# Performance work log

Measured on AMD Instinct MI355X. Metric: run time of the kernel, lower is better.

## Reference

```python
import jax, jax.numpy as jnp
import numpy as np

B, C, H, W = 8, 256, 128, 128
CQK = C // 8  # query/key channels from 1x1 conv
NEG = -jnp.inf


def setup_inputs() -> dict:
    key = jax.random.key(0)
    ks = jax.random.split(key, 9)
    s = 0.05
    return {
        "x1": jax.random.normal(ks[0], (B, C, H, W), jnp.float32),
        "x2": jax.random.normal(ks[1], (B, C, H, W), jnp.float32),
        "Wq": jax.random.normal(ks[2], (CQK, C), jnp.float32) * s,
        "bq": jax.random.normal(ks[3], (CQK,), jnp.float32) * s,
        "Wk": jax.random.normal(ks[4], (CQK, C), jnp.float32) * s,
        "bk": jax.random.normal(ks[5], (CQK,), jnp.float32) * s,
        "Wv": jax.random.normal(ks[6], (C, C), jnp.float32) * s,
        "bv": jax.random.normal(ks[7], (C,), jnp.float32) * s,
        "gamma": jnp.ones((1,), jnp.float32),
    }


def _topk_mask(e, k):
    # keep top-k entries along last axis, set the rest to -inf
    vals = jax.lax.top_k(e, k)[0]
    thr = vals[..., -1:]
    return jnp.where(e >= thr, e, NEG)


def reference(x1, x2, Wq, bq, Wk, bk, Wv, bv, gamma):
    b, c, h, w = x1.shape
    # 1x1 convs == per-pixel linear maps over channels
    q = jnp.einsum('bchw,oc->bohw', x1, Wq) + bq[None, :, None, None]
    k = jnp.einsum('bchw,oc->bohw', x2, Wk) + bk[None, :, None, None]
    v = jnp.einsum('bchw,oc->bohw', x2, Wv) + bv[None, :, None, None]

    # column (H-axis) scores: for pixel (h,w), attend over all h' in same column w
    eH = jnp.einsum('bchw,bcgw->bhwg', q, k)                     # (B,H,W,H)
    eye = jnp.eye(h, dtype=bool)[None, :, None, :]               # mask self on H-axis
    eH = jnp.where(eye, NEG, eH)
    # row (W-axis) scores: attend over all w' in same row h
    eW = jnp.einsum('bchw,bchv->bhwv', q, k)                     # (B,H,W,W)

    # top-k sparsification along each axis (keep top half)
    eH = _topk_mask(eH, h // 2)
    eW = _topk_mask(eW, w // 2)

    att = jax.nn.softmax(jnp.concatenate([eH, eW], axis=-1), axis=-1)  # (B,H,W,H+W)
    attH, attW = att[..., :h], att[..., h:]

    outH = jnp.einsum('bcgw,bhwg->bchw', v, attH)
    outW = jnp.einsum('bchv,bhwv->bchw', v, attW)
    return gamma[0] * (outH + outW) + x1
```

## Files before the change

### kernel.cpp

```cpp
#include <hip/hip_runtime.h>
#include <cstdint>
#include <cstddef>

#define HW 16384
#define NEGF (-__builtin_inff())

typedef unsigned short u16;
typedef _Float16 f16;
typedef _Float16 f16x8 __attribute__((ext_vector_type(8)));
typedef float f32x4 __attribute__((ext_vector_type(4)));

__device__ __forceinline__ unsigned fkey(float f) {
  unsigned b = __float_as_uint(f);
  return (b & 0x80000000u) ? ~b : (b | 0x80000000u);
}
__device__ __forceinline__ float funkey(unsigned u) {
  unsigned b = (u & 0x80000000u) ? (u ^ 0x80000000u) : ~u;
  return __uint_as_float(b);
}

__device__ __forceinline__ float h2f(u16 u) { f16 h; *(u16*)&h = u; return (float)h; }
__device__ __forceinline__ u16 f2h(float f) { f16 h = (f16)f; return *(u16*)&h; }

union i4h8 { int4 i; f16x8 h; };

__global__ __launch_bounds__(256) void pack_kernel(
    const float* __restrict__ Wq, const float* __restrict__ bq,
    const float* __restrict__ Wk, const float* __restrict__ bk,
    const float* __restrict__ Wv, const float* __restrict__ bv,
    u16* __restrict__ Wp, float* __restrict__ ball)
{
  int i = blockIdx.x * 256 + threadIdx.x;
  {
    int chunk = i / 10240;
    int r = i - chunk * 10240;
    int frag = r >> 9;
    int lane = (r >> 3) & 63;
    int j = i & 7;
    int o = frag * 16 + (lane & 15);
    int kk = chunk * 32 + (lane >> 4) * 8 + j;
    float wv_ = (o < 32) ? Wq[o * 256 + kk]
              : (o < 64) ? Wk[(o - 32) * 256 + kk]
                         : Wv[(o - 64) * 256 + kk];
    Wp[i] = f2h(wv_);
  }
  if (i < 320) {
    ball[i] = (i < 32) ? bq[i] : (i < 64) ? bk[i - 32] : bv[i - 64];
  }
}

__global__ __launch_bounds__(256) void proj_kernel(
    const float* __restrict__ x1, const float* __restrict__ x2,
    const u16* __restrict__ Wp, const float* __restrict__ ball,
    u16* __restrict__ q16, u16* __restrict__ k16, u16* __restrict__ v)
{
  __shared__ __align__(16) char smem[42496];
  u16* wlds = (u16*)smem;
  u16* xlds0 = (u16*)(smem + 20480);
  u16* xlds1 = (u16*)(smem + 24576);

  const int t = threadIdx.x;
  const int w = t >> 6, l = t & 63;
  const int l15 = l & 15, l4 = l >> 4;
  const int blk = blockIdx.x;
  const int b = blk >> 8;
  const int p0 = (blk & 255) << 6;

  f32x4 acc[5][4];
#pragma unroll
  for (int f = 0; f < 5; ++f) {
    f32x4 binit;
#pragma unroll
    for (int r = 0; r < 4; ++r)
      binit[r] = ball[(w * 5 + f) * 16 + l4 * 4 + r];
#pragma unroll
    for (int pf = 0; pf < 4; ++pf) acc[f][pf] = binit;
  }

  const float* xp = (w & 1) ? x2 : x1;
  const int ks_l = (w >> 1) * 16 + (l >> 5) * 8;
  const int px_w = (l & 31) * 2;
  char* xdst = (char*)((w & 1) ? xlds1 : xlds0);
  const int kgw = ks_l >> 3;
  const int offA = px_w * 64 + ((kgw ^ (px_w & 3)) << 4);
  const int offB = (px_w + 1) * 64 + ((kgw ^ ((px_w + 1) & 3)) << 4);

  const int prow = l15, kg2 = l4;
  const char* xsrc1 = (const char*)xlds0;
  const char* xsrc2 = (const char*)xlds1;

  for (int ch = 0; ch < 8; ++ch) {
    int4 wreg[5];
#pragma unroll
    for (int r = 0; r < 5; ++r)
      wreg[r] = *(const int4*)((const char*)Wp + ch * 20480 + (r * 256 + t) * 16);
    float2 xv[8];
    {
      size_t gbase = ((size_t)(b * 256 + ch * 32 + ks_l)) * HW + p0 + px_w;
#pragma unroll
      for (int i = 0; i < 8; ++i) xv[i] = *(const float2*)&xp[gbase + (size_t)i * HW];
    }
    __syncthreads();
#pragma unroll
    for (int r = 0; r < 5; ++r)
      *(int4*)((char*)wlds + (r * 256 + t) * 16) = wreg[r];
    {
      union { u16 h[8]; int4 v4; } pk0, pk1;
#pragma unroll
      for (int i = 0; i < 8; ++i) {
        pk0.h[i] = f2h(xv[i].x); pk1.h[i] = f2h(xv[i].y);
      }
      *(int4*)(xdst + offA) = pk0.v4;
      *(int4*)(xdst + offB) = pk1.v4;
    }
    __syncthreads();

    f16x8 af[5];
#pragma unroll
    for (int f = 0; f < 5; ++f)
      af[f] = *(const f16x8*)((const char*)wlds + (((w * 5 + f) * 64 + l) << 4));
    f16x8 bf[4];
#pragma unroll
    for (int pf = 0; pf < 4; ++pf) {
      int row = pf * 16 + prow;
      bf[pf] = *(const f16x8*)(xsrc2 + row * 64 + ((kg2 ^ (row & 3)) << 4));
    }
    if (w == 0) {
#pragma unroll
      for (int f = 2; f < 5; ++f)
#pragma unroll
        for (int pf = 0; pf < 4; ++pf)
          acc[f][pf] = __builtin_amdgcn_mfma_f32_16x16x32_f16(af[f], bf[pf], acc[f][pf], 0, 0, 0);
#pragma unroll
      for (int pf = 0; pf < 4; ++pf) {
        int row = pf * 16 + prow;
        bf[pf] = *(const f16x8*)(xsrc1 + row * 64 + ((kg2 ^ (row & 3)) << 4));
      }
#pragma unroll
      for (int f = 0; f < 2; ++f)
#pragma unroll
        for (int pf = 0; pf < 4; ++pf)
          acc[f][pf] = __builtin_amdgcn_mfma_f32_16x16x32_f16(af[f], bf[pf], acc[f][pf], 0, 0, 0);
    } else {
#pragma unroll
      for (int f = 0; f < 5; ++f)
#pragma unroll
        for (int pf = 0; pf < 4; ++pf)
          acc[f][pf] = __builtin_amdgcn_mfma_f32_16x16x32_f16(af[f], bf[pf], acc[f][pf], 0, 0, 0);
    }
  }

  __syncthreads();
  u16* vs2 = (u16*)smem;
  u16* qks = (u16*)(smem + 33280);
#pragma unroll
  for (int f = 0; f < 5; ++f) {
    int of = w * 5 + f;
    if (of >= 4) {
      int cb = (of - 4) * 16 + l4 * 4;
#pragma unroll
      for (int pf = 0; pf < 4; ++pf) {
        ushort4 h4;
        h4.x = f2h(acc[f][pf][0]); h4.y = f2h(acc[f][pf][1]);
        h4.z = f2h(acc[f][pf][2]); h4.w = f2h(acc[f][pf][3]);
        *(ushort4*)&vs2[(pf * 16 + l15) * 260 + cb] = h4;
      }
    } else {
      int ob = (of & 1) * 16 + l4 * 4;
      int selo = (of >> 1) * 2304;
#pragma unroll
      for (int pf = 0; pf < 4; ++pf) {
        ushort4 h4;
        h4.x = f2h(acc[f][pf][0]); h4.y = f2h(acc[f][pf][1]);
        h4.z = f2h(acc[f][pf][2]); h4.w = f2h(acc[f][pf][3]);
        *(ushort4*)&qks[selo + (pf * 16 + l15) * 36 + ob] = h4;
      }
    }
  }
  __syncthreads();
  {
    const int c = t;
    u16* dst = v + ((size_t)b * 256 + c) * HW + p0;
#pragma unroll
    for (int g8 = 0; g8 < 8; ++g8) {
      union { u16 h[8]; int4 i; } u;
#pragma unroll
      for (int j = 0; j < 8; ++j) u.h[j] = vs2[(g8 * 8 + j) * 260 + c];
      *(int4*)&dst[g8 * 8] = u.i;
    }
  }
  if (t < 128) {
    const int sel = t >> 6, px = t & 63;
    const unsigned long long* sp =
        (const unsigned long long*)(qks + sel * 2304 + px * 36);
    u16* dst = (sel ? k16 : q16) + ((size_t)b * HW + p0 + px) * 32;
    union { unsigned long long u[8]; int4 i4[4]; } buf;
#pragma unroll
    for (int j = 0; j < 8; ++j) buf.u[j] = sp[j];
#pragma unroll
    for (int j = 0; j < 4; ++j) *(int4*)&dst[j * 8] = buf.i4[j];
  }
}

__global__ __launch_bounds__(256) void transpose_b16(
    const u16* __restrict__ in, u16* __restrict__ out)
{
  __shared__ u16 s[32][33];
  const int plane = blockIdx.y;
  const int tw = blockIdx.x & 3, th = blockIdx.x >> 2;
  const u16* ip = in + (size_t)plane * HW;
  u16* op = out + (size_t)plane * HW;
  const int lx = threadIdx.x & 31, ly = threadIdx.x >> 5;
  const int r0 = th << 5, c0 = tw << 5;
#pragma unroll
  for (int r = 0; r < 4; ++r) s[ly + 8 * r][lx] = ip[(r0 + ly + 8 * r) * 128 + c0 + lx];
  __syncthreads();
#pragma unroll
  for (int r = 0; r < 4; ++r) op[(c0 + ly + 8 * r) * 128 + r0 + lx] = s[lx][ly + 8 * r];
}

__global__ __launch_bounds__(256) void transpose_c32(
    const u16* __restrict__ in, u16* __restrict__ out)
{
  const int b = blockIdx.y;
  const int tw = blockIdx.x & 7, th = blockIdx.x >> 3;
  const int lw = threadIdx.x & 15, lh = threadIdx.x >> 4;
  const int h = th * 16 + lh, wc = tw * 16 + lw;
  const u16* src = in + ((size_t)b * HW + h * 128 + wc) * 32;
  u16* dst = out + ((size_t)b * HW + wc * 128 + h) * 32;
  int4 v0 = *(const int4*)&src[0];
  int4 v1 = *(const int4*)&src[8];
  int4 v2 = *(const int4*)&src[16];
  int4 v3 = *(const int4*)&src[24];
  *(int4*)&dst[0] = v0;  *(int4*)&dst[8] = v1;
  *(int4*)&dst[16] = v2; *(int4*)&dst[24] = v3;
}

__global__ __launch_bounds__(256) void stats_kernel(
    const u16* __restrict__ qp, const u16* __restrict__ kp,
    float* __restrict__ thr_out, float* __restrict__ m_out, float* __restrict__ l_out,
    int diag)
{
  __shared__ float q_s[32][132];
  __shared__ float k_s[32][132];
  __shared__ float e_s[32][132];
  const int t = threadIdx.x;
  const int po = blockIdx.x, b = blockIdx.y;

  const u16* qt = qp + (size_t)(b * 128 + po) * 128 * 32;
  const u16* kt = kp + (size_t)(b * 128 + po) * 128 * 32;
#pragma unroll
  for (int r = 0; r < 2; ++r) {
    int idx = t * 8 + r * 2048;
    int h = idx >> 5, c0 = idx & 31;
    i4h8 qv; qv.i = *(const int4*)&qt[idx];
    i4h8 kv; kv.i = *(const int4*)&kt[idx];
#pragma unroll
    for (int j = 0; j < 8; ++j) {
      q_s[c0 + j][h] = (float)qv.h[j];
      k_s[c0 + j][h] = (float)kv.h[j];
    }
  }
  __syncthreads();

  const int hh = t >> 3;
  const int gg0 = (t & 7) << 4;
  const int wv = t >> 6, ln = t & 63;

  for (int h0 = 0; h0 < 128; h0 += 32) {
    float acc[16];
#pragma unroll
    for (int j = 0; j < 16; ++j) acc[j] = 0.0f;
#pragma unroll
    for (int c = 0; c < 32; ++c) {
      float qv = q_s[c][h0 + hh];
      float4 kv[4];
      kv[0] = *(const float4*)&k_s[c][gg0];
      kv[1] = *(const float4*)&k_s[c][gg0 + 4];
      kv[2] = *(const float4*)&k_s[c][gg0 + 8];
      kv[3] = *(const float4*)&k_s[c][gg0 + 12];
#pragma unroll
      for (int j4 = 0; j4 < 4; ++j4) {
        acc[j4 * 4 + 0] = fmaf(qv, kv[j4].x, acc[j4 * 4 + 0]);
        acc[j4 * 4 + 1] = fmaf(qv, kv[j4].y, acc[j4 * 4 + 1]);
        acc[j4 * 4 + 2] = fmaf(qv, kv[j4].z, acc[j4 * 4 + 2]);
        acc[j4 * 4 + 3] = fmaf(qv, kv[j4].w, acc[j4 * 4 + 3]);
      }
    }
    if (diag) {
      int h = h0 + hh;
#pragma unroll
      for (int j = 0; j < 16; ++j)
        if (gg0 + j == h) acc[j] = NEGF;
    }
#pragma unroll
    for (int j4 = 0; j4 < 4; ++j4)
      *(float4*)&e_s[hh][gg0 + j4 * 4] =
          make_float4(acc[j4 * 4 + 0], acc[j4 * 4 + 1], acc[j4 * 4 + 2], acc[j4 * 4 + 3]);
    __syncthreads();

    for (int rr = 0; rr < 8; ++rr) {
      int row = wv * 8 + rr;
      float e0 = e_s[row][ln], e1 = e_s[row][ln + 64];
      unsigned u0 = fkey(e0), u1 = fkey(e1);
      unsigned uthr = 0u;
      for (int bit = 31; bit >= 0; --bit) {
        unsigned cand = uthr | (1u << bit);
        int cnt = __popcll(__ballot(u0 >= cand)) + __popcll(__ballot(u1 >= cand));
        if (cnt >= 64) uthr = cand;
      }
      unsigned um = u0 > u1 ? u0 : u1;
#pragma unroll
      for (int off = 32; off; off >>= 1) {
        unsigned o = __shfl_xor(um, off);
        um = um > o ? um : o;
      }
      float m = funkey(um);
      float s = ((u0 >= uthr) ? __expf(e0 - m) : 0.0f) +
                ((u1 >= uthr) ? __expf(e1 - m) : 0.0f);
#pragma unroll
      for (int off = 32; off; off >>= 1) s += __shfl_xor(s, off);
      if (ln == 0) {
        size_t idx = ((size_t)b * 128 + po) * 128 + h0 + row;
        thr_out[idx] = __uint_as_float(uthr);
        m_out[idx] = m;
        l_out[idx] = s;
      }
    }
    __syncthreads();
  }
}

template <int DIAG>
__global__ __launch_bounds__(512) void out_mfma(
    const u16* __restrict__ q16, const u16* __restrict__ k16, const u16* __restrict__ vp,
    const float* __restrict__ thr_own, const float* __restrict__ m_own, const float* __restrict__ l_own,
    const float* __restrict__ m_oth, const float* __restrict__ l_oth,
    u16* __restrict__ outp)
{
  __shared__ __align__(16) char smem[50688];
  u16* q_s   = (u16*)smem;
  u16* k_s   = (u16*)(smem + 8192);
  u16* att_s = (u16*)(smem + 16384);
  float* m_s = (float*)(smem + 49152);
  float* il_s = (float*)(smem + 49664);
  unsigned* ut_s = (unsigned*)(smem + 50176);
  u16* stage = (u16*)smem;

  const int t = threadIdx.x;
  const int w = t >> 6, l = t & 63;
  const int l15 = l & 15, l4 = l >> 4;
  const int po = blockIdx.x, b = blockIdx.y;

  int4 vld[2][4];
#pragma unroll
  for (int nf = 0; nf < 2; ++nf) {
    int c = w * 32 + nf * 16 + l15;
    size_t vb = ((size_t)(b * 256 + c) * 128 + po) * 128 + l4 * 8;
#pragma unroll
    for (int ks = 0; ks < 4; ++ks)
      vld[nf][ks] = *(const int4*)&vp[vb + ks * 32];
  }

  {
    const u16* qt = q16 + (size_t)(b * 128 + po) * 128 * 32;
    const u16* kt = k16 + (size_t)(b * 128 + po) * 128 * 32;
    *(int4*)&q_s[t * 8] = *(const int4*)&qt[t * 8];
    *(int4*)&k_s[t * 8] = *(const int4*)&kt[t * 8];
  }
  if (t < 128) {
    size_t own = ((size_t)b * 128 + po) * 128 + t;
    size_t oth = ((size_t)b * 128 + t) * 128 + po;
    float ma = m_own[own], la = l_own[own];
    float mb = m_oth[oth], lb = l_oth[oth];
    float m = fmaxf(ma, mb);
    float lsum = la * __expf(ma - m) + lb * __expf(mb - m);
    m_s[t] = m;
    il_s[t] = 1.0f / lsum;
    ut_s[t] = __float_as_uint(thr_own[own]);
  }
  __syncthreads();

  f32x4 eacc[8];
#pragma unroll
  for (int nj = 0; nj < 8; ++nj) eacc[nj] = (f32x4){0.f, 0.f, 0.f, 0.f};
  {
    f16x8 aq = *(const f16x8*)&q_s[(w * 16 + l15) * 32 + l4 * 8];
#pragma unroll
    for (int nj = 0; nj < 8; ++nj) {
      f16x8 bk = *(const f16x8*)&k_s[(nj * 16 + l15) * 32 + l4 * 8];
      eacc[nj] = __builtin_amdgcn_mfma_f32_16x16x32_f16(aq, bk, eacc[nj], 0, 0, 0);
    }
  }

  {
    float mm[4], ii[4];
    unsigned uu[4];
#pragma unroll
    for (int r = 0; r < 4; ++r) {
      int i = w * 16 + l4 * 4 + r;
      mm[r] = m_s[i]; ii[r] = il_s[i]; uu[r] = ut_s[i];
    }
#pragma unroll
    for (int nj = 0; nj < 8; ++nj) {
      int j = nj * 16 + l15;
#pragma unroll
      for (int r = 0; r < 4; ++r) {
        int i = w * 16 + l4 * 4 + r;
        float e = eacc[nj][r];
        float a;
        if (DIAG && i == j) {
          a = 0.0f;
        } else {
          unsigned ue = fkey(e);
          a = (ue >= uu[r]) ? __expf(e - mm[r]) * ii[r] : 0.0f;
        }
        att_s[i * 128 + ((((j >> 3) ^ (i & 15)) << 3) | (j & 7))] = f2h(a);
      }
    }
  }
  __syncthreads();

  f32x4 acc[8][2];
#pragma unroll
  for (int mi = 0; mi < 8; ++mi)
#pragma unroll
    for (int nf = 0; nf < 2; ++nf) acc[mi][nf] = (f32x4){0.f, 0.f, 0.f, 0.f};

#pragma unroll
  for (int ks = 0; ks < 4; ++ks) {
    i4h8 bv0, bv1;
    bv0.i = vld[0][ks];
    bv1.i = vld[1][ks];
#pragma unroll
    for (int mi = 0; mi < 8; ++mi) {
      int i = mi * 16 + l15;
      int s = (ks * 4 + l4) ^ (i & 15);
      f16x8 pa = *(const f16x8*)&att_s[i * 128 + s * 8];
      acc[mi][0] = __builtin_amdgcn_mfma_f32_16x16x32_f16(pa, bv0.h, acc[mi][0], 0, 0, 0);
      acc[mi][1] = __builtin_amdgcn_mfma_f32_16x16x32_f16(pa, bv1.h, acc[mi][1], 0, 0, 0);
    }
  }

  __syncthreads();
#pragma unroll
  for (int rd = 0; rd < 2; ++rd) {
    if ((w >> 2) == rd) {
#pragma unroll
      for (int mi = 0; mi < 8; ++mi)
#pragma unroll
        for (int nf = 0; nf < 2; ++nf) {
          int cslot = (w & 3) * 32 + nf * 16 + l15;
          int i = mi * 16 + l4 * 4;
          ushort4 h4;
          h4.x = f2h(acc[mi][nf][0]); h4.y = f2h(acc[mi][nf][1]);
          h4.z = f2h(acc[mi][nf][2]); h4.w = f2h(acc[mi][nf][3]);
          *(ushort4*)&stage[cslot * 132 + i] = h4;
        }
    }
    __syncthreads();
    {
      const int cslot = t >> 2, seg = t & 3;
      const int c = rd * 128 + cslot;
      const unsigned long long* sp =
          (const unsigned long long*)(stage + cslot * 132 + seg * 32);
      u16* dst = outp + ((size_t)(b * 256 + c) * 128 + po) * 128 + seg * 32;
      union { unsigned long long u[8]; int4 i4[4]; } buf;
#pragma unroll
      for (int j = 0; j < 8; ++j) buf.u[j] = sp[j];
#pragma unroll
      for (int j = 0; j < 4; ++j) *(int4*)&dst[j * 8] = buf.i4[j];
    }
    if (rd == 0) __syncthreads();
  }
}

__global__ __launch_bounds__(256) void addT2_kernel(
    const u16* __restrict__ accW, const u16* __restrict__ accH,
    const float* __restrict__ x1, const float* __restrict__ gptr,
    float* __restrict__ out)
{
  __shared__ __align__(16) u16 hs[64][72];
  const int plane = blockIdx.y;
  const int th = blockIdx.x >> 1, tw = blockIdx.x & 1;
  const int h0 = th * 64, w0 = tw * 64;
  const float g = gptr[0];
  const int t = threadIdx.x;

  {
    int wr = t >> 2, seg = t & 3;
    const u16* src = accH + (size_t)plane * HW + (size_t)(w0 + wr) * 128 + h0 + seg * 16;
    int4 a = *(const int4*)&src[0];
    int4 b2 = *(const int4*)&src[8];
    *(int4*)&hs[wr][seg * 16] = a;
    *(int4*)&hs[wr][seg * 16 + 8] = b2;
  }
  __syncthreads();

  const int h = t & 63, wseg = t >> 6;
  size_t rbase = (size_t)plane * HW + (size_t)(h0 + h) * 128 + w0 + wseg * 16;
  const u16* wsrc = accW + rbase;
  const float* xsrc = x1 + rbase;
  float* osrc = out + rbase;
  union { int4 i4[2]; u16 hx[16]; } uw;
  uw.i4[0] = *(const int4*)&wsrc[0];
  uw.i4[1] = *(const int4*)&wsrc[8];
#pragma unroll
  for (int j4 = 0; j4 < 4; ++j4) {
    float4 xv = *(const float4*)&xsrc[j4 * 4];
    float4 o;
    o.x = g * (h2f(uw.hx[j4 * 4 + 0]) + h2f(hs[wseg * 16 + j4 * 4 + 0][h])) + xv.x;
    o.y = g * (h2f(uw.hx[j4 * 4 + 1]) + h2f(hs[wseg * 16 + j4 * 4 + 1][h])) + xv.y;
    o.z = g * (h2f(uw.hx[j4 * 4 + 2]) + h2f(hs[wseg * 16 + j4 * 4 + 2][h])) + xv.z;
    o.w = g * (h2f(uw.hx[j4 * 4 + 3]) + h2f(hs[wseg * 16 + j4 * 4 + 3][h])) + xv.w;
    *(float4*)&osrc[j4 * 4] = o;
  }
}

extern "C" void kernel_launch(void* const* d_in, const int* in_sizes, int n_in,
                              void* d_out, int out_size, void* d_ws, size_t ws_size,
                              hipStream_t stream)
{
  const float* x1 = (const float*)d_in[0];
  const float* x2 = (const float*)d_in[1];
  const float* Wq = (const float*)d_in[2];
  const float* bq = (const float*)d_in[3];
  const float* Wk = (const float*)d_in[4];
  const float* bk = (const float*)d_in[5];
  const float* Wv = (const float*)d_in[6];
  const float* bv = (const float*)d_in[7];
  const float* gm = (const float*)d_in[8];
  float* out = (float*)d_out;
  float* ws = (float*)d_ws;

  u16*   Wp    = (u16*)ws;
  float* ball  = ws + 81920;
  u16*   q16   = (u16*)(ws + 82304);
  u16*   k16   = q16 + 4194304;
  u16*   q16T  = k16 + 4194304;
  u16*   k16T  = q16T + 4194304;
  float* stats = (float*)(k16T + 4194304);
  u16*   v     = (u16*)(stats + 786432);
  u16*   vT    = v + 33554432;

  float* thrH = stats;
  float* mH   = stats + 131072;
  float* lH   = stats + 262144;
  float* thrW = stats + 393216;
  float* mW   = stats + 524288;
  float* lW   = stats + 655360;

  pack_kernel<<<320, 256, 0, stream>>>(Wq, bq, Wk, bk, Wv, bv, Wp, ball);
  proj_kernel<<<2048, 256, 0, stream>>>(x1, x2, Wp, ball, q16, k16, v);
  transpose_b16<<<dim3(16, 2048), 256, 0, stream>>>(v, vT);
  transpose_c32<<<dim3(64, 8), 256, 0, stream>>>(q16, q16T);
  transpose_c32<<<dim3(64, 8), 256, 0, stream>>>(k16, k16T);
  stats_kernel<<<dim3(128, 8), 256, 0, stream>>>(q16T, k16T, thrH, mH, lH, 1);
  stats_kernel<<<dim3(128, 8), 256, 0, stream>>>(q16, k16, thrW, mW, lW, 0);
  out_mfma<0><<<dim3(128, 8), 512, 0, stream>>>(
      q16, k16, v, thrW, mW, lW, mH, lH, v);
  out_mfma<1><<<dim3(128, 8), 512, 0, stream>>>(
      q16T, k16T, vT, thrH, mH, lH, mW, lW, vT);
  addT2_kernel<<<dim3(4, 2048), 256, 0, stream>>>(v, vT, x1, gm, out);
}
```

Baseline: 837.6 us.

## Coalesce global stores and shrink LDS staging in projection, attention and add kernels

Projection epilogue now stages V in two 128-channel halves, which shrinks shared memory and may raise occupancy, and remaps threads so each 16-byte store covers contiguous pixels. Q/K writes use padded LDS rows and coalesced 16-byte chunks. The attention output staging pad changes from 132 to 136, and stores are remapped so adjacent threads write contiguous row segments. The final add kernel remaps threads so each row is read and written contiguously across lanes, at the cost of an extra barrier in the projection epilogue.

```diff
diff --git a/kernel.cpp b/kernel.cpp
--- a/kernel.cpp
+++ b/kernel.cpp
@@ -54,7 +54,7 @@
     const u16* __restrict__ Wp, const float* __restrict__ ball,
     u16* __restrict__ q16, u16* __restrict__ k16, u16* __restrict__ v)
 {
-  __shared__ __align__(16) char smem[42496];
+  __shared__ __align__(16) char smem[28672];
   u16* wlds = (u16*)smem;
   u16* xlds0 = (u16*)(smem + 20480);
   u16* xlds1 = (u16*)(smem + 24576);
@@ -151,54 +151,67 @@
   }
 
   __syncthreads();
-  u16* vs2 = (u16*)smem;
-  u16* qks = (u16*)(smem + 33280);
+  u16* vs_half = (u16*)smem;
+  u16* qks = (u16*)(smem + 16896);
+
 #pragma unroll
   for (int f = 0; f < 5; ++f) {
     int of = w * 5 + f;
-    if (of >= 4) {
-      int cb = (of - 4) * 16 + l4 * 4;
+    if (of < 4) {
+      int ob = (of & 1) * 16 + l4 * 4;
+      int selo = (of >> 1) * 2560;
 #pragma unroll
       for (int pf = 0; pf < 4; ++pf) {
         ushort4 h4;
         h4.x = f2h(acc[f][pf][0]); h4.y = f2h(acc[f][pf][1]);
         h4.z = f2h(acc[f][pf][2]); h4.w = f2h(acc[f][pf][3]);
-        *(ushort4*)&vs2[(pf * 16 + l15) * 260 + cb] = h4;
-      }
-    } else {
-      int ob = (of & 1) * 16 + l4 * 4;
-      int selo = (of >> 1) * 2304;
-#pragma unroll
-      for (int pf = 0; pf < 4; ++pf) {
-        ushort4 h4;
-        h4.x = f2h(acc[f][pf][0]); h4.y = f2h(acc[f][pf][1]);
-        h4.z = f2h(acc[f][pf][2]); h4.w = f2h(acc[f][pf][3]);
-        *(ushort4*)&qks[selo + (pf * 16 + l15) * 36 + ob] = h4;
-      }
-    }
-  }
-  __syncthreads();
-  {
-    const int c = t;
-    u16* dst = v + ((size_t)b * 256 + c) * HW + p0;
-#pragma unroll
-    for (int g8 = 0; g8 < 8; ++g8) {
+        *(ushort4*)&qks[selo + (pf * 16 + l15) * 40 + ob] = h4;
+      }
+    }
+  }
+
+#pragma unroll
+  for (int rd = 0; rd < 2; ++rd) {
+#pragma unroll
+    for (int f = 0; f < 5; ++f) {
+      int of = w * 5 + f;
+      if (of >= 4) {
+        int cb = (of - 4) * 16 + l4 * 4;
+        if ((cb >> 7) == rd) {
+          int cl = cb & 127;
+#pragma unroll
+          for (int pf = 0; pf < 4; ++pf) {
+            ushort4 h4;
+            h4.x = f2h(acc[f][pf][0]); h4.y = f2h(acc[f][pf][1]);
+            h4.z = f2h(acc[f][pf][2]); h4.w = f2h(acc[f][pf][3]);
+            *(ushort4*)&vs_half[(pf * 16 + l15) * 132 + cl] = h4;
+          }
+        }
+      }
+    }
+    __syncthreads();
+#pragma unroll
+    for (int n = 0; n < 4; ++n) {
+      int cl = n * 32 + (t >> 3);
+      int pxo = (t & 7) * 8;
       union { u16 h[8]; int4 i; } u;
 #pragma unroll
-      for (int j = 0; j < 8; ++j) u.h[j] = vs2[(g8 * 8 + j) * 260 + c];
-      *(int4*)&dst[g8 * 8] = u.i;
-    }
-  }
-  if (t < 128) {
-    const int sel = t >> 6, px = t & 63;
-    const unsigned long long* sp =
-        (const unsigned long long*)(qks + sel * 2304 + px * 36);
-    u16* dst = (sel ? k16 : q16) + ((size_t)b * HW + p0 + px) * 32;
-    union { unsigned long long u[8]; int4 i4[4]; } buf;
-#pragma unroll
-    for (int j = 0; j < 8; ++j) buf.u[j] = sp[j];
-#pragma unroll
-    for (int j = 0; j < 4; ++j) *(int4*)&dst[j * 8] = buf.i4[j];
+      for (int j = 0; j < 8; ++j) u.h[j] = vs_half[(pxo + j) * 132 + cl];
+      *(int4*)&v[((size_t)b * 256 + rd * 128 + cl) * HW + p0 + pxo] = u.i;
+    }
+    if (rd == 0) {
+      if (t < 128) {
+        int sel = t >> 6, l2 = t & 63;
+        u16* dst16 = sel ? k16 : q16;
+#pragma unroll
+        for (int r = 0; r < 4; ++r) {
+          int px = r * 16 + (l2 >> 2), seg = l2 & 3;
+          int4 d = *(const int4*)&qks[sel * 2560 + px * 40 + seg * 8];
+          *(int4*)&dst16[((size_t)b * HW + p0 + px) * 32 + seg * 8] = d;
+        }
+      }
+      __syncthreads();
+    }
   }
 }
 
@@ -455,21 +468,16 @@
           ushort4 h4;
           h4.x = f2h(acc[mi][nf][0]); h4.y = f2h(acc[mi][nf][1]);
           h4.z = f2h(acc[mi][nf][2]); h4.w = f2h(acc[mi][nf][3]);
-          *(ushort4*)&stage[cslot * 132 + i] = h4;
+          *(ushort4*)&stage[cslot * 136 + i] = h4;
         }
     }
     __syncthreads();
-    {
-      const int cslot = t >> 2, seg = t & 3;
-      const int c = rd * 128 + cslot;
-      const unsigned long long* sp =
-          (const unsigned long long*)(stage + cslot * 132 + seg * 32);
-      u16* dst = outp + ((size_t)(b * 256 + c) * 128 + po) * 128 + seg * 32;
-      union { unsigned long long u[8]; int4 i4[4]; } buf;
-#pragma unroll
-      for (int j = 0; j < 8; ++j) buf.u[j] = sp[j];
-#pragma unroll
-      for (int j = 0; j < 4; ++j) *(int4*)&dst[j * 8] = buf.i4[j];
+#pragma unroll
+    for (int n = 0; n < 4; ++n) {
+      int cslot = n * 32 + (t >> 4);
+      int io = (t & 15) * 8;
+      int4 d = *(const int4*)&stage[cslot * 136 + io];
+      *(int4*)&outp[((size_t)(b * 256 + rd * 128 + cslot) * 128 + po) * 128 + io] = d;
     }
     if (rd == 0) __syncthreads();
   }
@@ -497,23 +505,19 @@
   }
   __syncthreads();
 
-  const int h = t & 63, wseg = t >> 6;
-  size_t rbase = (size_t)plane * HW + (size_t)(h0 + h) * 128 + w0 + wseg * 16;
-  const u16* wsrc = accW + rbase;
-  const float* xsrc = x1 + rbase;
-  float* osrc = out + rbase;
-  union { int4 i4[2]; u16 hx[16]; } uw;
-  uw.i4[0] = *(const int4*)&wsrc[0];
-  uw.i4[1] = *(const int4*)&wsrc[8];
-#pragma unroll
-  for (int j4 = 0; j4 < 4; ++j4) {
-    float4 xv = *(const float4*)&xsrc[j4 * 4];
+#pragma unroll
+  for (int n = 0; n < 4; ++n) {
+    int h = n * 16 + (t >> 4);
+    int wo = (t & 15) * 4;
+    size_t rbase = (size_t)plane * HW + (size_t)(h0 + h) * 128 + w0 + wo;
+    ushort4 aw = *(const ushort4*)&accW[rbase];
+    float4 xv = *(const float4*)&x1[rbase];
     float4 o;
-    o.x = g * (h2f(uw.hx[j4 * 4 + 0]) + h2f(hs[wseg * 16 + j4 * 4 + 0][h])) + xv.x;
-    o.y = g * (h2f(uw.hx[j4 * 4 + 1]) + h2f(hs[wseg * 16 + j4 * 4 + 1][h])) + xv.y;
-    o.z = g * (h2f(uw.hx[j4 * 4 + 2]) + h2f(hs[wseg * 16 + j4 * 4 + 2][h])) + xv.z;
-    o.w = g * (h2f(uw.hx[j4 * 4 + 3]) + h2f(hs[wseg * 16 + j4 * 4 + 3][h])) + xv.w;
-    *(float4*)&osrc[j4 * 4] = o;
+    o.x = g * (h2f(aw.x) + h2f(hs[wo + 0][h])) + xv.x;
+    o.y = g * (h2f(aw.y) + h2f(hs[wo + 1][h])) + xv.y;
+    o.z = g * (h2f(aw.z) + h2f(hs[wo + 2][h])) + xv.z;
+    o.w = g * (h2f(aw.w) + h2f(hs[wo + 3][h])) + xv.w;
+    *(float4*)&out[rbase] = o;
   }
 }
 
```

After: 764.7 us. 8.7% less time.
